# Performance work log

Hardware: AMD Instinct MI355X
Metric: run time of the kernel (lower is better)

## Reference

```python
import jax, jax.numpy as jnp
import numpy as np

TAU = 2.0
V_TH = 1.0
SG_ALPHA = 4.0  # spikingjelly surrogate.Sigmoid default alpha
BN_EPS = 1e-5


@jax.custom_vjp
def spike_fn(x):
    # Heaviside with sigmoid surrogate gradient
    return (x >= 0).astype(x.dtype)

def _spike_fwd(x):
    return spike_fn(x), x

def _spike_bwd(x, g):
    s = jax.nn.sigmoid(SG_ALPHA * x)
    return (g * SG_ALPHA * s * (1.0 - s),)

spike_fn.defvjp(_spike_fwd, _spike_bwd)


def lif_multistep(x):
    # x: [T, B, C, N]; hard reset to 0, detach_reset=True, v_reset=0
    def step(v, xt):
        v = v + (xt - v) / TAU
        s = spike_fn(v - V_TH)
        v = v * (1.0 - jax.lax.stop_gradient(s))
        return v, s
    _, spikes = jax.lax.scan(step, jnp.zeros_like(x[0]), x)
    return spikes


def batchnorm(h, gamma, beta):
    # h: [TB, C']; training-mode BN over batch dim
    mu = h.mean(axis=0)
    var = h.var(axis=0)
    return (h - mu) * jax.lax.rsqrt(var + BN_EPS) * gamma + beta


def setup_inputs() -> dict:
    key = jax.random.key(0)
    ks = jax.random.split(key, 3)
    T, B, C, N, Cr = 4, 16, 512, 1024, 64
    x = jax.random.uniform(ks[0], (T, B, C, N), dtype=jnp.float32)
    w1 = jax.random.normal(ks[1], (Cr, C), dtype=jnp.float32) * (1.0 / np.sqrt(C))
    w2 = jax.random.normal(ks[2], (C, Cr), dtype=jnp.float32) * (1.0 / np.sqrt(Cr))
    return {
        "x": x,
        "w1": w1, "b1": jnp.zeros((Cr,), jnp.float32),
        "gamma1": jnp.ones((Cr,), jnp.float32), "beta1": jnp.zeros((Cr,), jnp.float32),
        "w2": w2, "b2": jnp.zeros((C,), jnp.float32),
        "gamma2": jnp.ones((C,), jnp.float32), "beta2": jnp.zeros((C,), jnp.float32),
    }


def reference(x, w1, b1, gamma1, beta1, w2, b2, gamma2, beta2):
    T, B, C, N = x.shape
    s = lif_multistep(x)                      # [T, B, C, N] spikes in {0,1}
    g = s.reshape(T * B, C, N).mean(axis=-1)  # GAP -> [TB, C]
    h = g @ w1.T + b1                         # 1x1 conv -> [TB, Cr]
    h = batchnorm(h, gamma1, beta1)
    h = h @ w2.T + b2                         # 1x1 conv -> [TB, C]
    h = batchnorm(h, gamma2, beta2)
    return h.reshape(T, B, C, 1)
```

## Files before the change

kernel.cpp:

```cpp
#include <hip/hip_runtime.h>

#define T_  4
#define B_  16
#define C_  512
#define N_  1024
#define CR_ 64

static constexpr float BN_EPS = 1e-5f;

typedef float f4_t __attribute__((ext_vector_type(4)));

__global__ __launch_bounds__(256) void lif_gap_kernel(
    const float* __restrict__ x, float* __restrict__ g) {
    const int blk = blockIdx.x;
    const int b   = blk >> 9;
    const int c   = blk & (C_ - 1);
    const int tid = threadIdx.x;
    const size_t plane = (size_t)B_ * C_ * N_;
    const float* __restrict__ xp = x + ((size_t)(b * C_ + c)) * N_ + (size_t)tid * 4;

    f4_t v = (f4_t)(0.f);
    int cnt[T_];
#pragma unroll
    for (int t = 0; t < T_; ++t) {
        const f4_t* p = (const f4_t*)(xp + (size_t)t * plane);
        const f4_t xv = __builtin_nontemporal_load(p);
        v.x = 0.5f * (v.x + xv.x);
        v.y = 0.5f * (v.y + xv.y);
        v.z = 0.5f * (v.z + xv.z);
        v.w = 0.5f * (v.w + xv.w);
        const unsigned long long m0 = __ballot(v.x >= 1.0f);
        const unsigned long long m1 = __ballot(v.y >= 1.0f);
        const unsigned long long m2 = __ballot(v.z >= 1.0f);
        const unsigned long long m3 = __ballot(v.w >= 1.0f);
        cnt[t] = (int)(__popcll(m0) + __popcll(m1) + __popcll(m2) + __popcll(m3));
        v.x = (v.x >= 1.0f) ? 0.f : v.x;
        v.y = (v.y >= 1.0f) ? 0.f : v.y;
        v.z = (v.z >= 1.0f) ? 0.f : v.z;
        v.w = (v.w >= 1.0f) ? 0.f : v.w;
    }

    __shared__ int lds[4 * T_];
    const int wave = tid >> 6;
    const int lane = tid & 63;
    if (lane == 0) {
#pragma unroll
        for (int t = 0; t < T_; ++t) lds[wave * T_ + t] = cnt[t];
    }
    __syncthreads();
    if (tid < T_) {
        const int tot = lds[0 * T_ + tid] + lds[1 * T_ + tid] +
                        lds[2 * T_ + tid] + lds[3 * T_ + tid];
        g[((size_t)(tid * B_ + b)) * C_ + c] = (float)tot * (1.0f / N_);
    }
}

__global__ __launch_bounds__(256) void fc1_bn_kernel(
    const float* __restrict__ g,  const float* __restrict__ w1,
    const float* __restrict__ b1, const float* __restrict__ gamma1,
    const float* __restrict__ beta1, float* __restrict__ h1) {
    const int j    = blockIdx.x;
    const int tid  = threadIdx.x;
    const int lane = tid & 63;
    const int wave = tid >> 6;
    __shared__ float rowval[64];

    const float* __restrict__ w1r = w1 + (size_t)j * C_;
    for (int i = wave; i < 64; i += 4) {
        float p = 0.f;
        const float* __restrict__ gr = g + (size_t)i * C_;
#pragma unroll
        for (int m = 0; m < C_ / 64; ++m) {
            const int k = lane + 64 * m;
            p += gr[k] * w1r[k];
        }
#pragma unroll
        for (int off = 32; off >= 1; off >>= 1) p += __shfl_xor(p, off, 64);
        if (lane == 0) rowval[i] = p + b1[j];
    }
    __syncthreads();
    if (tid < 64) {
        const float v = rowval[tid];
        float s  = v;
        float s2 = v * v;
#pragma unroll
        for (int off = 32; off >= 1; off >>= 1) {
            s  += __shfl_xor(s,  off, 64);
            s2 += __shfl_xor(s2, off, 64);
        }
        const float mu  = s * (1.f / 64.f);
        const float var = s2 * (1.f / 64.f) - mu * mu;
        h1[(size_t)tid * CR_ + j] =
            (v - mu) * rsqrtf(var + BN_EPS) * gamma1[j] + beta1[j];
    }
}

__global__ __launch_bounds__(64) void fc2_bn_kernel(
    const float* __restrict__ h1, const float* __restrict__ w2,
    const float* __restrict__ b2, const float* __restrict__ gamma2,
    const float* __restrict__ beta2, float* __restrict__ out) {
    const int j = blockIdx.x;
    const int i = threadIdx.x;
    const float* __restrict__ w2r = w2 + (size_t)j * CR_;
    const float* __restrict__ hr  = h1 + (size_t)i * CR_;
    float v = b2[j];
#pragma unroll
    for (int k = 0; k < CR_; ++k) v += hr[k] * w2r[k];

    float s  = v;
    float s2 = v * v;
#pragma unroll
    for (int off = 32; off >= 1; off >>= 1) {
        s  += __shfl_xor(s,  off, 64);
        s2 += __shfl_xor(s2, off, 64);
    }
    const float mu  = s * (1.f / 64.f);
    const float var = s2 * (1.f / 64.f) - mu * mu;
    out[(size_t)i * C_ + j] =
        (v - mu) * rsqrtf(var + BN_EPS) * gamma2[j] + beta2[j];
}

extern "C" void kernel_launch(void* const* d_in, const int* in_sizes, int n_in,
                              void* d_out, int out_size, void* d_ws, size_t ws_size,
                              hipStream_t stream) {
    const float* x      = (const float*)d_in[0];
    const float* w1     = (const float*)d_in[1];
    const float* b1     = (const float*)d_in[2];
    const float* gamma1 = (const float*)d_in[3];
    const float* beta1  = (const float*)d_in[4];
    const float* w2     = (const float*)d_in[5];
    const float* b2     = (const float*)d_in[6];
    const float* gamma2 = (const float*)d_in[7];
    const float* beta2  = (const float*)d_in[8];
    float* out = (float*)d_out;

    float* g  = (float*)d_ws;
    float* h1 = g + 64 * C_;

    lif_gap_kernel<<<B_ * C_, 256, 0, stream>>>(x, g);
    fc1_bn_kernel<<<CR_, 256, 0, stream>>>(g, w1, b1, gamma1, beta1, h1);
    fc2_bn_kernel<<<C_, 64, 0, stream>>>(h1, w2, b2, gamma2, beta2, out);
}
```

Baseline: 207.7 us.

## Fuse FC1 and FC2 kernels with a global atomic flag barrier

Merges the two small FC+BN kernels into one 128-block launch. The first 64 blocks compute h1 and increment a global counter, and all blocks spin on that counter before running FC2 out of an LDS copy of h1. The LIF kernel now resets the flag and issues all four time-step loads up front. This removes one launch and its inter-kernel gap, but it depends on all blocks being co-resident to avoid deadlock and adds spin-wait overhead.

```diff
diff --git a/kernel.cpp b/kernel.cpp
--- a/kernel.cpp
+++ b/kernel.cpp
@@ -11,24 +11,28 @@
 typedef float f4_t __attribute__((ext_vector_type(4)));
 
 __global__ __launch_bounds__(256) void lif_gap_kernel(
-    const float* __restrict__ x, float* __restrict__ g) {
+    const float* __restrict__ x, float* __restrict__ g, int* __restrict__ flag) {
     const int blk = blockIdx.x;
+    const int tid = threadIdx.x;
+    if (blk == 0 && tid == 0) *flag = 0;
     const int b   = blk >> 9;
     const int c   = blk & (C_ - 1);
-    const int tid = threadIdx.x;
     const size_t plane = (size_t)B_ * C_ * N_;
     const float* __restrict__ xp = x + ((size_t)(b * C_ + c)) * N_ + (size_t)tid * 4;
+
+    f4_t xv[T_];
+#pragma unroll
+    for (int t = 0; t < T_; ++t)
+        xv[t] = __builtin_nontemporal_load((const f4_t*)(xp + (size_t)t * plane));
 
     f4_t v = (f4_t)(0.f);
     int cnt[T_];
 #pragma unroll
     for (int t = 0; t < T_; ++t) {
-        const f4_t* p = (const f4_t*)(xp + (size_t)t * plane);
-        const f4_t xv = __builtin_nontemporal_load(p);
-        v.x = 0.5f * (v.x + xv.x);
-        v.y = 0.5f * (v.y + xv.y);
-        v.z = 0.5f * (v.z + xv.z);
-        v.w = 0.5f * (v.w + xv.w);
+        v.x = 0.5f * (v.x + xv[t].x);
+        v.y = 0.5f * (v.y + xv[t].y);
+        v.z = 0.5f * (v.z + xv[t].z);
+        v.w = 0.5f * (v.w + xv[t].w);
         const unsigned long long m0 = __ballot(v.x >= 1.0f);
         const unsigned long long m1 = __ballot(v.y >= 1.0f);
         const unsigned long long m2 = __ballot(v.z >= 1.0f);
@@ -55,60 +59,83 @@
     }
 }
 
-__global__ __launch_bounds__(256) void fc1_bn_kernel(
+__global__ __launch_bounds__(256) void fc_fused_kernel(
     const float* __restrict__ g,  const float* __restrict__ w1,
     const float* __restrict__ b1, const float* __restrict__ gamma1,
-    const float* __restrict__ beta1, float* __restrict__ h1) {
-    const int j    = blockIdx.x;
+    const float* __restrict__ beta1,
+    const float* __restrict__ w2, const float* __restrict__ b2,
+    const float* __restrict__ gamma2, const float* __restrict__ beta2,
+    float* __restrict__ h1, int* __restrict__ flag,
+    float* __restrict__ out) {
     const int tid  = threadIdx.x;
     const int lane = tid & 63;
     const int wave = tid >> 6;
     __shared__ float rowval[64];
+    __shared__ float h1s[64][65];
 
-    const float* __restrict__ w1r = w1 + (size_t)j * C_;
-    for (int i = wave; i < 64; i += 4) {
-        float p = 0.f;
-        const float* __restrict__ gr = g + (size_t)i * C_;
+    if (blockIdx.x < CR_) {
+        const int j = blockIdx.x;
+        const float* __restrict__ w1r = w1 + (size_t)j * C_;
+        const int sub = lane >> 4;
+        const int kl  = lane & 15;
 #pragma unroll
-        for (int m = 0; m < C_ / 64; ++m) {
-            const int k = lane + 64 * m;
-            p += gr[k] * w1r[k];
+        for (int it = 0; it < 4; ++it) {
+            const int r = wave * 16 + it * 4 + sub;
+            const float* __restrict__ gr = g + (size_t)r * C_;
+            float p0 = 0.f, p1 = 0.f;
+#pragma unroll
+            for (int m = 0; m < 16; ++m) {
+                const int k = kl + 32 * m;
+                p0 += gr[k]      * w1r[k];
+                p1 += gr[k + 16] * w1r[k + 16];
+            }
+            float p = p0 + p1;
+            p += __shfl_xor(p, 1, 64);
+            p += __shfl_xor(p, 2, 64);
+            p += __shfl_xor(p, 4, 64);
+            p += __shfl_xor(p, 8, 64);
+            if (kl == 0) rowval[r] = p + b1[j];
         }
+        __syncthreads();
+        if (tid < 64) {
+            const float vv = rowval[tid];
+            float s = vv, s2 = vv * vv;
 #pragma unroll
-        for (int off = 32; off >= 1; off >>= 1) p += __shfl_xor(p, off, 64);
-        if (lane == 0) rowval[i] = p + b1[j];
+            for (int off = 32; off >= 1; off >>= 1) {
+                s  += __shfl_xor(s,  off, 64);
+                s2 += __shfl_xor(s2, off, 64);
+            }
+            const float mu  = s * (1.f / 64.f);
+            const float var = s2 * (1.f / 64.f) - mu * mu;
+            h1[(size_t)tid * CR_ + j] =
+                (vv - mu) * rsqrtf(var + BN_EPS) * gamma1[j] + beta1[j];
+        }
+        __syncthreads();
+        if (tid == 0) {
+            __threadfence();
+            atomicAdd(flag, 1);
+        }
+    }
+
+    if (tid == 0) {
+        while (__hip_atomic_load(flag, __ATOMIC_RELAXED, __HIP_MEMORY_SCOPE_AGENT) < CR_)
+            __builtin_amdgcn_s_sleep(8);
+        __threadfence();
     }
     __syncthreads();
-    if (tid < 64) {
-        const float v = rowval[tid];
-        float s  = v;
-        float s2 = v * v;
+
+    for (int e = tid; e < 64 * 64; e += 256)
+        h1s[e >> 6][e & 63] = h1[e];
+    __syncthreads();
+
+    const int j2 = blockIdx.x * 4 + wave;
+    const float* __restrict__ w2r = w2 + (size_t)j2 * CR_;
+    float v = b2[j2];
 #pragma unroll
-        for (int off = 32; off >= 1; off >>= 1) {
-            s  += __shfl_xor(s,  off, 64);
-            s2 += __shfl_xor(s2, off, 64);
-        }
-        const float mu  = s * (1.f / 64.f);
-        const float var = s2 * (1.f / 64.f) - mu * mu;
-        h1[(size_t)tid * CR_ + j] =
-            (v - mu) * rsqrtf(var + BN_EPS) * gamma1[j] + beta1[j];
-    }
-}
+    for (int k = 0; k < CR_; ++k)
+        v += h1s[lane][k] * w2r[k];
 
-__global__ __launch_bounds__(64) void fc2_bn_kernel(
-    const float* __restrict__ h1, const float* __restrict__ w2,
-    const float* __restrict__ b2, const float* __restrict__ gamma2,
-    const float* __restrict__ beta2, float* __restrict__ out) {
-    const int j = blockIdx.x;
-    const int i = threadIdx.x;
-    const float* __restrict__ w2r = w2 + (size_t)j * CR_;
-    const float* __restrict__ hr  = h1 + (size_t)i * CR_;
-    float v = b2[j];
-#pragma unroll
-    for (int k = 0; k < CR_; ++k) v += hr[k] * w2r[k];
-
-    float s  = v;
-    float s2 = v * v;
+    float s = v, s2 = v * v;
 #pragma unroll
     for (int off = 32; off >= 1; off >>= 1) {
         s  += __shfl_xor(s,  off, 64);
@@ -116,8 +143,8 @@
     }
     const float mu  = s * (1.f / 64.f);
     const float var = s2 * (1.f / 64.f) - mu * mu;
-    out[(size_t)i * C_ + j] =
-        (v - mu) * rsqrtf(var + BN_EPS) * gamma2[j] + beta2[j];
+    out[(size_t)lane * C_ + j2] =
+        (v - mu) * rsqrtf(var + BN_EPS) * gamma2[j2] + beta2[j2];
 }
 
 extern "C" void kernel_launch(void* const* d_in, const int* in_sizes, int n_in,
@@ -134,10 +161,12 @@
     const float* beta2  = (const float*)d_in[8];
     float* out = (float*)d_out;
 
-    float* g  = (float*)d_ws;
-    float* h1 = g + 64 * C_;
+    float* g    = (float*)d_ws;
+    float* h1   = g + 64 * C_;
+    int*   flag = (int*)(h1 + 64 * CR_);
 
-    lif_gap_kernel<<<B_ * C_, 256, 0, stream>>>(x, g);
-    fc1_bn_kernel<<<CR_, 256, 0, stream>>>(g, w1, b1, gamma1, beta1, h1);
-    fc2_bn_kernel<<<C_, 64, 0, stream>>>(h1, w2, b2, gamma2, beta2, out);
+    lif_gap_kernel<<<B_ * C_, 256, 0, stream>>>(x, g, flag);
+    fc_fused_kernel<<<128, 256, 0, stream>>>(g, w1, b1, gamma1, beta1,
+                                             w2, b2, gamma2, beta2,
+                                             h1, flag, out);
 }
```

After: 218.9 us. 1.05x slower.
